# Kernel optimization log

Measured on AMD Instinct MI355X. Metric: run time of the kernel, lower is better.

Reference implementation:

```python
import jax, jax.numpy as jnp
import numpy as np

N, D, M = 65536, 1024, 32768

def setup_inputs() -> dict:
    key = jax.random.key(0)
    k1, k2, k3, k4, k5 = jax.random.split(key, 5)
    var = jax.random.randint(k1, (N, D), -128, 128, dtype=jnp.int8)
    var_scale = jax.random.uniform(k2, (1,), jnp.float32) * 0.02 + 0.01
    indices = jax.random.randint(k3, (M, D), 0, N, dtype=jnp.int32)
    updates = (jax.random.normal(k4, (M, D)) ).astype(jnp.float16)
    smooth_scales = (jax.random.uniform(k5, (D,)) + 0.5).astype(jnp.float16)
    return {"var": var, "var_scale": var_scale, "indices": indices,
            "updates": updates, "smooth_scales": smooth_scales}

def reference(var, var_scale, indices, updates, smooth_scales):
    # dequantize int8 var with fp32 scale
    out = var.astype(jnp.float32) * var_scale  # [N, D]
    # smooth-scale the updates, promote to fp32
    upd = (updates * smooth_scales).astype(jnp.float32)  # [M, D]
    # torch scatter_add_ along axis 0: out[indices[i,j], j] += upd[i,j]
    cols = jnp.arange(out.shape[1])[None, :]  # [1, D] broadcasts vs [M, D] indices
    out = out.at[indices, cols].add(upd)
    # global abs-max -> dynamic requantization to int8
    max_val = jnp.max(jnp.abs(out))
    new_scale = max_val / 127.0
    y = jnp.clip(jnp.round(out / new_scale), -128, 127).astype(jnp.int8)
    return (y, out, new_scale[None])
```

## Files before the change

kernel.cpp:

```cpp
#include <hip/hip_runtime.h>
#include <hip/hip_fp16.h>

#define N_ROWS 65536
#define D_COLS 1024
#define M_ROWS 32768
#define QROWS  16384

using u32 = unsigned int;
using u16 = unsigned short;
typedef float f32x4 __attribute__((ext_vector_type(4)));
typedef int   i32x4 __attribute__((ext_vector_type(4)));

__global__ void init_ws_k(u32* ws) {
    if (threadIdx.x == 0 && blockIdx.x == 0) ws[0] = 0u;
}

__global__ __launch_bounds__(256) void t_idx_upd_k(const int* __restrict__ idx,
                                                   const float* __restrict__ upd,
                                                   const float* __restrict__ scl,
                                                   u16* __restrict__ idxT,
                                                   __half* __restrict__ updT) {
    __shared__ u32   sidx[64][65];
    __shared__ float supd[64][65];
    const int swz = (int)(blockIdx.x & 7) * 1024 + (int)(blockIdx.x >> 3);
    const int i0 = (swz & 511) * 64;
    const int j0 = (swz >> 9) * 64;
    const int t = threadIdx.x;

    {
        const int rr = t >> 2, c4 = t & 3;
        const int*   ip = idx + (size_t)(i0 + rr) * D_COLS + j0;
        const float* up = upd + (size_t)(i0 + rr) * D_COLS + j0;
        #pragma unroll
        for (int cq = 0; cq < 4; ++cq) {
            const int jc = cq * 16 + c4 * 4;
            const i32x4 iv = __builtin_nontemporal_load((const i32x4*)(ip + jc));
            const f32x4 uv = __builtin_nontemporal_load((const f32x4*)(up + jc));
            sidx[rr][jc] = (u32)iv.x; sidx[rr][jc+1] = (u32)iv.y;
            sidx[rr][jc+2] = (u32)iv.z; sidx[rr][jc+3] = (u32)iv.w;
            supd[rr][jc] = uv.x; supd[rr][jc+1] = uv.y;
            supd[rr][jc+2] = uv.z; supd[rr][jc+3] = uv.w;
        }
    }
    __syncthreads();

    {
        const int jj = t >> 2, seg = t & 3;
        const __half hs = __float2half(scl[j0 + jj]);
        u32 wi[8], wh[8];
        #pragma unroll
        for (int p = 0; p < 8; ++p) {
            const int r = seg * 16 + 2 * p;
            const u32 a = sidx[r][jj] & 0xffffu, b = sidx[r + 1][jj] & 0xffffu;
            wi[p] = a | (b << 16);
            const __half2 h2 = __halves2half2(__hmul(__float2half(supd[r][jj]), hs),
                                              __hmul(__float2half(supd[r + 1][jj]), hs));
            wh[p] = *reinterpret_cast<const u32*>(&h2);
        }
        u16* di = idxT + (size_t)(j0 + jj) * M_ROWS + i0 + seg * 16;
        __half* dh = updT + (size_t)(j0 + jj) * M_ROWS + i0 + seg * 16;
        ((uint4*)di)[0] = uint4{wi[0], wi[1], wi[2], wi[3]};
        ((uint4*)di)[1] = uint4{wi[4], wi[5], wi[6], wi[7]};
        ((uint4*)dh)[0] = uint4{wh[0], wh[1], wh[2], wh[3]};
        ((uint4*)dh)[1] = uint4{wh[4], wh[5], wh[6], wh[7]};
    }
}

__global__ __launch_bounds__(1024) void scatter_q_k(const u16* __restrict__ idxT,
                                                    const __half* __restrict__ updT,
                                                    __half* __restrict__ sumT) {
    __shared__ float acc[QROWS];
    const int bid = (blockIdx.x & 7) * 512 + (blockIdx.x >> 3);
    const int j = bid >> 2;
    const int h = bid & 3;
    const int tid = threadIdx.x;

    float4* acc4 = (float4*)acc;
    for (int t = tid; t < QROWS / 4; t += 1024) acc4[t] = float4{0.f, 0.f, 0.f, 0.f};

    const int4* ip4 = (const int4*)(idxT + (size_t)j * M_ROWS);
    const int4* up4 = (const int4*)(updT + (size_t)j * M_ROWS);
    __syncthreads();

    #pragma unroll
    for (int k = 0; k < 4; ++k) {
        const int t = k * 1024 + tid;
        const int4 iv = ip4[t];
        const int4 uv = up4[t];
        const u32 iw[4] = {(u32)iv.x, (u32)iv.y, (u32)iv.z, (u32)iv.w};
        const u32 uw[4] = {(u32)uv.x, (u32)uv.y, (u32)uv.z, (u32)uv.w};
        #pragma unroll
        for (int e = 0; e < 4; ++e) {
            const int r0 = iw[e] & 0xffff, r1 = iw[e] >> 16;
            const __half2 h2 = *reinterpret_cast<const __half2*>(&uw[e]);
            if ((r0 >> 14) == h) atomicAdd(&acc[r0 & (QROWS - 1)], __half2float(__low2half(h2)));
            if ((r1 >> 14) == h) atomicAdd(&acc[r1 & (QROWS - 1)], __half2float(__high2half(h2)));
        }
    }
    __syncthreads();

    __half2* dst = (__half2*)(sumT + (size_t)j * N_ROWS + h * QROWS);
    for (int t = tid; t < QROWS / 2; t += 1024)
        dst[t] = __floats2half2_rn(acc[2 * t], acc[2 * t + 1]);
}

__global__ __launch_bounds__(256) void finalize_k(const int* __restrict__ var,
                                                  const __half* __restrict__ sumT,
                                                  const float* __restrict__ var_scale,
                                                  float* __restrict__ outf,
                                                  u32* __restrict__ ws) {
    __shared__ float sm[64][68];
    __shared__ float wmax[4];
    const int swz = (int)(blockIdx.x & 7) * 2048 + (int)(blockIdx.x >> 3);
    const int r0 = (swz & 1023) * 64;
    const int j0 = (swz >> 10) * 64;
    const int tid = threadIdx.x;
    const float s = var_scale[0];

    {
        const int jj = tid >> 2, seg = tid & 3;
        const __half* colp = sumT + (size_t)(j0 + jj) * N_ROWS + r0 + seg * 16;
        #pragma unroll
        for (int q = 0; q < 2; ++q) {
            const uint4 w = ((const uint4*)colp)[q];
            const u32 wv[4] = {w.x, w.y, w.z, w.w};
            #pragma unroll
            for (int i = 0; i < 4; ++i) {
                const __half2 hh = *reinterpret_cast<const __half2*>(&wv[i]);
                const float2 f = __half22float2(hh);
                const int rr = seg * 16 + q * 8 + i * 2;
                sm[rr][jj] = f.x;
                sm[rr + 1][jj] = f.y;
            }
        }
    }
    __syncthreads();

    float m = 0.f;
    #pragma unroll
    for (int k = 0; k < 4; ++k) {
        const int l = k * 256 + tid;
        const int rr = l >> 4, c4 = l & 15;
        const i32x4 v = __builtin_nontemporal_load(
            (const i32x4*)(var + (size_t)(r0 + rr) * D_COLS + j0) + c4);
        const float4 sv = *(const float4*)&sm[rr][c4 * 4];
        float4 o;
        o.x = (float)v.x * s + sv.x;
        o.y = (float)v.y * s + sv.y;
        o.z = (float)v.z * s + sv.z;
        o.w = (float)v.w * s + sv.w;
        ((float4*)(outf + (size_t)(r0 + rr) * D_COLS + j0))[c4] = o;
        m = fmaxf(m, fmaxf(fmaxf(fabsf(o.x), fabsf(o.y)),
                           fmaxf(fabsf(o.z), fabsf(o.w))));
    }
    for (int off = 32; off; off >>= 1) m = fmaxf(m, __shfl_xor(m, off));
    if ((tid & 63) == 0) wmax[tid >> 6] = m;
    __syncthreads();
    if (tid == 0) {
        m = fmaxf(fmaxf(wmax[0], wmax[1]), fmaxf(wmax[2], wmax[3]));
        atomicMax(ws, __float_as_uint(m));
    }
}

__global__ __launch_bounds__(256) void quant_k(const float4* __restrict__ outf4,
                                               f32x4* __restrict__ y4,
                                               const u32* __restrict__ ws,
                                               float* __restrict__ scale_out, int n4) {
    const float mx = __uint_as_float(ws[0]);
    const float inv = 127.0f / mx;
    int gid = blockIdx.x * 256 + threadIdx.x;
    if (gid == 0) scale_out[0] = mx / 127.0f;
    const int stride = gridDim.x * 256;
    for (int i = gid; i < n4; i += stride) {
        float4 v = outf4[i];
        f32x4 o;
        o.x = fminf(fmaxf(rintf(v.x * inv), -128.f), 127.f);
        o.y = fminf(fmaxf(rintf(v.y * inv), -128.f), 127.f);
        o.z = fminf(fmaxf(rintf(v.z * inv), -128.f), 127.f);
        o.w = fminf(fmaxf(rintf(v.w * inv), -128.f), 127.f);
        __builtin_nontemporal_store(o, &y4[i]);
    }
}

extern "C" void kernel_launch(void* const* d_in, const int* in_sizes, int n_in,
                              void* d_out, int out_size, void* d_ws, size_t ws_size,
                              hipStream_t stream) {
    const int*   var       = (const int*)d_in[0];
    const float* var_scale = (const float*)d_in[1];
    const int*   idx       = (const int*)d_in[2];
    const float* upd       = (const float*)d_in[3];
    const float* scl       = (const float*)d_in[4];

    float* y    = (float*)d_out;
    float* outf = y + (size_t)N_ROWS * D_COLS;
    float* scale_out = y + 2 * (size_t)N_ROWS * D_COLS;

    char* scratch = (char*)y;
    u16*    idxT = (u16*)scratch;
    __half* updT = (__half*)(scratch + (size_t)67108864);
    __half* sumT = (__half*)(scratch + (size_t)134217728);
    u32* ws = (u32*)d_ws;

    const int n4 = N_ROWS * D_COLS / 4;

    init_ws_k<<<1, 64, 0, stream>>>(ws);
    t_idx_upd_k<<<8192, 256, 0, stream>>>(idx, upd, scl, idxT, updT);
    scatter_q_k<<<4096, 1024, 0, stream>>>(idxT, updT, sumT);
    finalize_k<<<16384, 256, 0, stream>>>(var, sumT, var_scale, outf, ws);
    quant_k<<<4096, 256, 0, stream>>>((const float4*)outf, (f32x4*)y, ws, scale_out, n4);
}
```

Baseline: 569.2 us.

## Use unsafeAtomicAdd for LDS accumulation and tile quant kernel like finalize

New measurement: 576.8 us. About the same (+1.3%).

```diff
diff --git a/kernel.cpp b/kernel.cpp
--- a/kernel.cpp
+++ b/kernel.cpp
@@ -93,8 +93,10 @@
         for (int e = 0; e < 4; ++e) {
             const int r0 = iw[e] & 0xffff, r1 = iw[e] >> 16;
             const __half2 h2 = *reinterpret_cast<const __half2*>(&uw[e]);
-            if ((r0 >> 14) == h) atomicAdd(&acc[r0 & (QROWS - 1)], __half2float(__low2half(h2)));
-            if ((r1 >> 14) == h) atomicAdd(&acc[r1 & (QROWS - 1)], __half2float(__high2half(h2)));
+            if ((r0 >> 14) == h)
+                unsafeAtomicAdd(&acc[r0 & (QROWS - 1)], __half2float(__low2half(h2)));
+            if ((r1 >> 14) == h)
+                unsafeAtomicAdd(&acc[r1 & (QROWS - 1)], __half2float(__high2half(h2)));
         }
     }
     __syncthreads();
@@ -162,23 +164,29 @@
     }
 }
 
-__global__ __launch_bounds__(256) void quant_k(const float4* __restrict__ outf4,
-                                               f32x4* __restrict__ y4,
+__global__ __launch_bounds__(256) void quant_k(const float* __restrict__ outf,
+                                               float* __restrict__ y,
                                                const u32* __restrict__ ws,
-                                               float* __restrict__ scale_out, int n4) {
+                                               float* __restrict__ scale_out) {
     const float mx = __uint_as_float(ws[0]);
     const float inv = 127.0f / mx;
-    int gid = blockIdx.x * 256 + threadIdx.x;
-    if (gid == 0) scale_out[0] = mx / 127.0f;
-    const int stride = gridDim.x * 256;
-    for (int i = gid; i < n4; i += stride) {
-        float4 v = outf4[i];
+    const int swz = (int)(blockIdx.x & 7) * 2048 + (int)(blockIdx.x >> 3);
+    const int r0 = (swz & 1023) * 64;
+    const int j0 = (swz >> 10) * 64;
+    const int tid = threadIdx.x;
+    if (blockIdx.x == 0 && tid == 0) scale_out[0] = mx / 127.0f;
+    #pragma unroll
+    for (int k = 0; k < 4; ++k) {
+        const int l = k * 256 + tid;
+        const int rr = l >> 4, c4 = l & 15;
+        const size_t off = (size_t)(r0 + rr) * D_COLS + j0 + c4 * 4;
+        const float4 v = *(const float4*)(outf + off);
         f32x4 o;
         o.x = fminf(fmaxf(rintf(v.x * inv), -128.f), 127.f);
         o.y = fminf(fmaxf(rintf(v.y * inv), -128.f), 127.f);
         o.z = fminf(fmaxf(rintf(v.z * inv), -128.f), 127.f);
         o.w = fminf(fmaxf(rintf(v.w * inv), -128.f), 127.f);
-        __builtin_nontemporal_store(o, &y4[i]);
+        __builtin_nontemporal_store(o, (f32x4*)(y + off));
     }
 }
 
@@ -201,11 +209,9 @@
     __half* sumT = (__half*)(scratch + (size_t)134217728);
     u32* ws = (u32*)d_ws;
 
-    const int n4 = N_ROWS * D_COLS / 4;
-
     init_ws_k<<<1, 64, 0, stream>>>(ws);
     t_idx_upd_k<<<8192, 256, 0, stream>>>(idx, upd, scl, idxT, updT);
     scatter_q_k<<<4096, 1024, 0, stream>>>(idxT, updT, sumT);
     finalize_k<<<16384, 256, 0, stream>>>(var, sumT, var_scale, outf, ws);
-    quant_k<<<4096, 256, 0, stream>>>((const float4*)outf, (f32x4*)y, ws, scale_out, n4);
-}
+    quant_k<<<16384, 256, 0, stream>>>(outf, y, ws, scale_out);
+}
```
